# Optimization experiments

Hardware: AMD Instinct MI355X
Metric: run time of the kernel (lower is better)

The kernel has to match this reference:

```python
import jax, jax.numpy as jnp
import numpy as np

B, S, HID = 1, 4096, 2048
NH, NKV, D = 16, 4, 128
BLK, M, K_TOP = 64, 32, 8
THETA = 10000.0
NEG = jnp.float32(-1e9)


def setup_inputs() -> dict:
    key = jax.random.key(0)
    ks = jax.random.split(key, 6)
    s = 0.02
    return {
        "hidden_states": jax.random.normal(ks[0], (B, S, HID), jnp.float32),
        "position_ids": jnp.arange(S, dtype=jnp.int32)[None, :],
        "Wq": jax.random.normal(ks[1], (HID, NH * D), jnp.float32) * s,
        "Wk": jax.random.normal(ks[2], (HID, NKV * D), jnp.float32) * s,
        "Wv": jax.random.normal(ks[3], (HID, NKV * D), jnp.float32) * s,
        "Wo": jax.random.normal(ks[4], (NH * D, HID), jnp.float32) * s,
        # seeded random-sign (Hadamard-style) sketch projection, non-trainable buffer
        "H_sketch": jnp.sign(jax.random.normal(ks[5], (D, M), jnp.float32)) / jnp.sqrt(jnp.float32(M)),
    }


def _rot_half(x):
    x1, x2 = x[..., : D // 2], x[..., D // 2 :]
    return jnp.concatenate([-x2, x1], axis=-1)


def reference(hidden_states, position_ids, Wq, Wk, Wv, Wo, H_sketch):
    # QKV projections -> [B, heads, S, D]
    q = (hidden_states @ Wq).reshape(B, S, NH, D).transpose(0, 2, 1, 3)
    k = (hidden_states @ Wk).reshape(B, S, NKV, D).transpose(0, 2, 1, 3)
    v = (hidden_states @ Wv).reshape(B, S, NKV, D).transpose(0, 2, 1, 3)

    # RoPE
    inv_freq = 1.0 / (THETA ** (jnp.arange(0, D, 2, dtype=jnp.float32) / D))
    freqs = position_ids.astype(jnp.float32)[:, :, None] * inv_freq[None, None, :]
    emb = jnp.concatenate([freqs, freqs], axis=-1)  # [B, S, D]
    cos, sin = jnp.cos(emb)[:, None], jnp.sin(emb)[:, None]  # [B, 1, S, D]
    q = q * cos + _rot_half(q) * sin
    k = k * cos + _rot_half(k) * sin

    # GQA repeat kv heads
    rep = NH // NKV
    k = jnp.repeat(k, rep, axis=1)
    v = jnp.repeat(v, rep, axis=1)

    nblk = S // BLK
    # Hadamard-sketch projections, block-mean pooled -> [B, NH, nblk, M]
    Sq = jnp.einsum("bhsd,dm->bhsm", q, H_sketch).reshape(B, NH, nblk, BLK, M).mean(axis=3)
    Sk = jnp.einsum("bhsd,dm->bhsm", k, H_sketch).reshape(B, NH, nblk, BLK, M).mean(axis=3)

    # Block-level sketch scores, causal at block granularity, diagonal forced in
    bs = jnp.einsum("bhim,bhjm->bhij", Sq, Sk)
    blk_causal = jnp.tril(jnp.ones((nblk, nblk), dtype=bool))
    bs = jnp.where(blk_causal, bs, NEG)
    bs = jnp.where(jnp.eye(nblk, dtype=bool), jnp.float32(1e9), bs)
    _, idx = jax.lax.top_k(bs, K_TOP)  # [B, NH, nblk, K_TOP]

    # Gather selected K/V blocks -> [B, NH, nblk, K_TOP, BLK, D]
    K5 = k.reshape(B, NH, nblk, BLK, D)
    V5 = v.reshape(B, NH, nblk, BLK, D)
    gidx = idx[..., None, None]
    Kg = jnp.take_along_axis(K5[:, :, None], gidx, axis=3)
    Vg = jnp.take_along_axis(V5[:, :, None], gidx, axis=3)

    # Block-sparse scores [B, NH, nblk, BLK, K_TOP, BLK]
    Qb = q.reshape(B, NH, nblk, BLK, D)
    scores = jnp.einsum("bhnqd,bhnkcd->bhnqkc", Qb, Kg) / jnp.sqrt(jnp.float32(D))

    # Token-level causal mask over gathered keys
    qpos = jnp.arange(nblk)[:, None] * BLK + jnp.arange(BLK)[None, :]  # [nblk, BLK]
    kpos = idx[..., None] * BLK + jnp.arange(BLK)  # [B, NH, nblk, K_TOP, BLK]
    mask = kpos[:, :, :, None] <= qpos[None, None, :, :, None, None]
    scores = jnp.where(mask, scores, NEG)

    probs = jax.nn.softmax(scores.reshape(B, NH, nblk, BLK, K_TOP * BLK), axis=-1)
    probs = probs.reshape(scores.shape)

    out = jnp.einsum("bhnqkc,bhnkcd->bhnqd", probs, Vg)
    out = out.reshape(B, NH, S, D).transpose(0, 2, 1, 3).reshape(B, S, NH * D)
    return out @ Wo
```

## Files before the change

kernel.cpp:

```cpp
#include <hip/hip_runtime.h>
#include <hip/hip_bf16.h>

#define S_LEN 4096
#define HID 2048
#define NH 16
#define NKV 4
#define HD 128
#define MSK 32
#define KTOP 8
#define NBLK 64
#define NEGV -1000000000.0f
#define SENT -3.0e38f

typedef __hip_bfloat16 bf16;
typedef __attribute__((ext_vector_type(8))) short short8;
typedef __attribute__((ext_vector_type(4))) float f32x4;


__device__ __forceinline__ unsigned short f2b(float v) {
    __hip_bfloat16 h = __float2bfloat16(v);
    return *reinterpret_cast<unsigned short*>(&h);
}
__device__ __forceinline__ float b2f(unsigned short u) {
    return __bfloat162float(*reinterpret_cast<__hip_bfloat16*>(&u));
}
__device__ __forceinline__ void gl16(const void* g, void* l) {
    __builtin_amdgcn_global_load_lds(
        (const __attribute__((address_space(1))) void*)g,
        (__attribute__((address_space(3))) void*)l, 16, 0, 0);
}

__global__ __launch_bounds__(256) void prepass(
    const float* __restrict__ Wq, const float* __restrict__ Wk,
    const float* __restrict__ Wv, const float* __restrict__ Wo,
    const float* __restrict__ A,
    bf16* __restrict__ WtqH, bf16* __restrict__ WtqL,
    bf16* __restrict__ WtkH, bf16* __restrict__ WtkL,
    bf16* __restrict__ WtvH, bf16* __restrict__ WtoH,
    bf16* __restrict__ AhiT, bf16* __restrict__ AloT,
    int nA) {
    __shared__ __align__(16) float LsArena[64 * 68];
    const int t = threadIdx.x;
    int bx = blockIdx.x;

    if (bx < nA) {
        const int rb = bx >> 6, kt = bx & 63;
        char* DH = (char*)AhiT + ((size_t)rb * 64 + kt) * 8192;
        char* DL = (char*)AloT + ((size_t)rb * 64 + kt) * 8192;
#pragma unroll
        for (int i = 0; i < 2; i++) {
            const int task = t + i * 256;
            const int row = task >> 2, lq = task & 3;
            const float* ap = &A[(size_t)(rb * 128 + row) * HID + kt * 32 + lq * 8];
            const float4 v0 = *(const float4*)ap;
            const float4 v1 = *(const float4*)(ap + 4);
            const float f[8] = {v0.x, v0.y, v0.z, v0.w, v1.x, v1.y, v1.z, v1.w};
            alignas(16) unsigned short hh[8], lo[8];
#pragma unroll
            for (int j = 0; j < 8; j++) {
                hh[j] = f2b(f[j]);
                lo[j] = f2b(f[j] - b2f(hh[j]));
            }
            const size_t off = (size_t)(((row * 4 + lq) ^ (row & 7))) * 16;
            *(uint4*)(DH + off) = *(const uint4*)hh;
            *(uint4*)(DL + off) = *(const uint4*)lo;
        }
        return;
    }
    bx -= nA;

    if (bx < 1536) {
        const int u = bx >> 6, kt = bx & 63, k0 = kt * 32;
        const float* W; char* TH; char* TL; int Nd, n0; bool hasLo;
        if (u < 16)      { W = Wq; TH = (char*)WtqH + (size_t)u * 524288;        TL = (char*)WtqL + (size_t)u * 524288; Nd = 2048; n0 = u * 128; hasLo = true; }
        else if (u < 20) { W = Wk; TH = (char*)WtkH + (size_t)(u - 16) * 524288; TL = (char*)WtkL + (size_t)(u - 16) * 524288; Nd = 512; n0 = (u - 16) * 128; hasLo = true; }
        else             { W = Wv; TH = (char*)WtvH + (size_t)(u - 20) * 524288; TL = nullptr; Nd = 512; n0 = (u - 20) * 128; hasLo = false; }
        float(*Lw)[132] = (float(*)[132])LsArena;
#pragma unroll
        for (int i = 0; i < 4; i++) {
            const int task = t + i * 256;
            const int k = task >> 5, c4 = task & 31;
            *(float4*)&Lw[k][c4 * 4] = *(const float4*)&W[(size_t)(k0 + k) * Nd + n0 + c4 * 4];
        }
        __syncthreads();
#pragma unroll
        for (int i = 0; i < 2; i++) {
            const int task = t + i * 256;
            const int col = task >> 2, lq = task & 3;
            alignas(16) unsigned short hh[8], lo[8];
#pragma unroll
            for (int j = 0; j < 8; j++) {
                const float x = Lw[lq * 8 + j][col];
                hh[j] = f2b(x);
                lo[j] = f2b(x - b2f(hh[j]));
            }
            const size_t off = (size_t)kt * 8192 + (size_t)(((col * 4 + lq) ^ (col & 7))) * 16;
            *(uint4*)(TH + off) = *(const uint4*)hh;
            if (hasLo) *(uint4*)(TL + off) = *(const uint4*)lo;
        }
        return;
    }
    bx -= 1536;

    {
        const int n0 = (bx >> 5) * 64, k0 = (bx & 31) * 64;
        float(*Ls)[68] = (float(*)[68])LsArena;
        {
            const int kk = t >> 2, c0 = (t & 3) * 16;
#pragma unroll
            for (int i = 0; i < 4; i++)
                *(float4*)&Ls[kk][c0 + i * 4] =
                    *(const float4*)&Wo[(size_t)(k0 + kk) * HID + n0 + c0 + i * 4];
        }
        __syncthreads();
        const int c = t >> 2, ks = (t & 3) * 16;
        alignas(16) unsigned short hh[16];
#pragma unroll
        for (int j = 0; j < 16; j++) hh[j] = f2b(Ls[ks + j][c]);
        unsigned short* TH = (unsigned short*)WtoH;
        const size_t db = (size_t)(n0 + c) * HID + k0 + ks;
        *(uint4*)&TH[db + 0] = *(const uint4*)&hh[0];
        *(uint4*)&TH[db + 8] = *(const uint4*)&hh[8];
    }
}

__global__ __launch_bounds__(256, 3) void proj4(
    const float* __restrict__ A,
    const bf16* __restrict__ AhiT_, const bf16* __restrict__ AloT_,
    const bf16* __restrict__ WtqH_, const bf16* __restrict__ WtqL_,
    const bf16* __restrict__ WtkH_, const bf16* __restrict__ WtkL_,
    const bf16* __restrict__ WtvH_,
    const int* __restrict__ pos_ids, const float* __restrict__ H,
    bf16* __restrict__ qf, bf16* __restrict__ kf, bf16* __restrict__ vfT,
    float* __restrict__ Sq, float* __restrict__ Sk) {
    const int u = blockIdx.x;
    const int rb = blockIdx.y;
    const bool isQ = (u < 16);
    const bool isV = (u >= 20);
    const bool np3 = !isV;
    const int h = isQ ? u : (isV ? (u - 20) : (u - 16));
    const char* WHb = (const char*)(isQ ? WtqH_ : (isV ? WtvH_ : WtkH_)) + (size_t)h * 524288;
    const char* WLb = (const char*)(isQ ? WtqL_ : WtkL_) + (size_t)h * 524288;
    const char* AHb = (const char*)AhiT_;
    const char* ALb = (const char*)AloT_;
    bf16* __restrict__ Xout = isQ ? qf : kf;
    float* __restrict__ Sout = isQ ? Sq : Sk;
    const int Nd = isQ ? (NH * HD) : (NKV * HD);

    const int m0g = rb * 128;
    const int t = threadIdx.x;
    const int w = t >> 6, L = t & 63;
    const int lm = L & 15, lq = L >> 4;

    __shared__ __align__(16) char arena[34816];
    __shared__ float red[4][128];
    char* Wh_s = arena;
    char* Wl_s = arena + 8192;
    char* Ah_s = arena + 16384;
    char* Al_s = arena + 24576;

    f32x4 acc[2][8];
#pragma unroll
    for (int mt = 0; mt < 2; mt++)
#pragma unroll
        for (int nt = 0; nt < 8; nt++) acc[mt][nt] = (f32x4){0.f, 0.f, 0.f, 0.f};

    for (int kt = 0; kt < 64; kt++) {
        __syncthreads();
        const size_t tW = (size_t)kt * 8192;
#pragma unroll
        for (int i = 0; i < 2; i++) {
            const int so = (w * 2 + i) * 1024;
            gl16(WHb + tW + so + L * 16, Wh_s + so);
            if (np3) gl16(WLb + tW + so + L * 16, Wl_s + so);
        }
        if (AHb) {
            const size_t tA = ((size_t)rb * 64 + kt) * 8192;
#pragma unroll
            for (int i = 0; i < 2; i++) {
                const int so = (w * 2 + i) * 1024;
                gl16(AHb + tA + so + L * 16, Ah_s + so);
                if (np3) gl16(ALb + tA + so + L * 16, Al_s + so);
            }
        } else {
            const int k0 = kt * 32;
#pragma unroll
            for (int i = 0; i < 2; i++) {
                const int task = t + i * 256;
                const int row = task >> 2, q2 = task & 3;
                const float* ap = &A[(size_t)(m0g + row) * HID + k0 + q2 * 8];
                const float4 v0 = *(const float4*)ap;
                const float4 v1 = *(const float4*)(ap + 4);
                const float f[8] = {v0.x, v0.y, v0.z, v0.w, v1.x, v1.y, v1.z, v1.w};
                alignas(16) unsigned short hh[8], lo[8];
#pragma unroll
                for (int j = 0; j < 8; j++) {
                    hh[j] = f2b(f[j]);
                    if (np3) lo[j] = f2b(f[j] - b2f(hh[j]));
                }
                const int ch = ((row * 4 + q2) ^ (row & 7)) * 16;
                *(uint4*)(Ah_s + ch) = *(const uint4*)hh;
                if (np3) *(uint4*)(Al_s + ch) = *(const uint4*)lo;
            }
        }
        __syncthreads();
        const int xr = lm & 7;
        short8 ah[2], al[2];
#pragma unroll
        for (int mt = 0; mt < 2; mt++) {
            const int rowA = w * 32 + mt * 16 + lm;
            const int cA = (((rowA * 4 + lq) ^ xr)) * 16;
            ah[mt] = *(const short8*)(Ah_s + cA);
            if (np3) al[mt] = *(const short8*)(Al_s + cA);
        }
#pragma unroll
        for (int nt = 0; nt < 8; nt++) {
            const int rowW = nt * 16 + lm;
            const int cW = (((rowW * 4 + lq) ^ xr)) * 16;
            const short8 bh = *(const short8*)(Wh_s + cW);
#pragma unroll
            for (int mt = 0; mt < 2; mt++)
                acc[mt][nt] = __builtin_amdgcn_mfma_f32_16x16x32_bf16(ah[mt], bh, acc[mt][nt], 0, 0, 0);
            if (np3) {
                const short8 bl = *(const short8*)(Wl_s + cW);
#pragma unroll
                for (int mt = 0; mt < 2; mt++) {
                    acc[mt][nt] = __builtin_amdgcn_mfma_f32_16x16x32_bf16(ah[mt], bl, acc[mt][nt], 0, 0, 0);
                    acc[mt][nt] = __builtin_amdgcn_mfma_f32_16x16x32_bf16(al[mt], bh, acc[mt][nt], 0, 0, 0);
                }
            }
        }
    }

    if (isV) {
        __syncthreads();
        unsigned short(*Tv)[136] = (unsigned short(*)[136])arena;
#pragma unroll
        for (int mt = 0; mt < 2; mt++) {
            const int rbs = w * 32 + mt * 16 + lq * 4;
#pragma unroll
            for (int rr = 0; rr < 4; rr++)
#pragma unroll
                for (int nt = 0; nt < 8; nt++)
                    Tv[nt * 16 + lm][rbs + rr] = f2b(acc[mt][nt][rr]);
        }
        __syncthreads();
        const int col = t >> 1, rh = (t & 1) * 64;
        bf16* dst = &vfT[((size_t)h * HD + col) * S_LEN + m0g + rh];
#pragma unroll
        for (int u2 = 0; u2 < 8; u2++)
            *(uint4*)&dst[u2 * 8] = *(const uint4*)&Tv[col][rh + u2 * 8];
        return;
    }

    {
        float invf[4];
#pragma unroll
        for (int c4 = 0; c4 < 4; c4++) {
            const int jj = c4 * 16 + lm;
            invf[c4] = 1.0f / powf(10000.0f, (float)jj * (1.0f / 64.0f));
        }
#pragma unroll
        for (int mt = 0; mt < 2; mt++) {
            const int rbase = w * 32 + mt * 16 + lq * 4;
#pragma unroll
            for (int rr = 0; rr < 4; rr++) {
                const float p = (float)pos_ids[m0g + rbase + rr];
#pragma unroll
                for (int c4 = 0; c4 < 4; c4++) {
                    const float fr = p * invf[c4];
                    float sv, cv;
                    sincosf(fr, &sv, &cv);
                    const float x1 = acc[mt][c4][rr];
                    const float x2 = acc[mt][c4 + 4][rr];
                    acc[mt][c4][rr]     = x1 * cv - x2 * sv;
                    acc[mt][c4 + 4][rr] = x2 * cv + x1 * sv;
                }
            }
        }
    }

    float cs[8];
#pragma unroll
    for (int nt = 0; nt < 8; nt++) cs[nt] = 0.f;
#pragma unroll
    for (int mt = 0; mt < 2; mt++) {
        const int rbase = w * 32 + mt * 16 + lq * 4;
#pragma unroll
        for (int rr = 0; rr < 4; rr++) {
            bf16* dst = &Xout[(size_t)(m0g + rbase + rr) * Nd + h * HD + lm];
#pragma unroll
            for (int nt = 0; nt < 8; nt++) {
                const float v = acc[mt][nt][rr];
                dst[nt * 16] = __float2bfloat16(v);
                cs[nt] += v;
            }
        }
    }
#pragma unroll
    for (int nt = 0; nt < 8; nt++) {
        cs[nt] += __shfl_xor(cs[nt], 16);
        cs[nt] += __shfl_xor(cs[nt], 32);
    }
    if (lq == 0) {
#pragma unroll
        for (int nt = 0; nt < 8; nt++) red[w][nt * 16 + lm] = cs[nt];
    }
    __syncthreads();
    if (t < 64) {
        const int b = t >> 5, m = t & 31;
        float s = 0.f;
        for (int d = 0; d < 128; d++)
            s += (red[b * 2][d] + red[b * 2 + 1][d]) * H[d * MSK + m];
        Sout[((size_t)h * NBLK + (m0g >> 6) + b) * MSK + m] = s * (1.0f / 64.0f);
    }
}

__global__ __launch_bounds__(256, 3) void proj_rope_sketch(
    const float* __restrict__ A, const float* __restrict__ Wq,
    const float* __restrict__ Wk, const float* __restrict__ Wv,
    const int* __restrict__ pos_ids, const float* __restrict__ H,
    bf16* __restrict__ qf, bf16* __restrict__ kf, bf16* __restrict__ vf,
    float* __restrict__ Sq, float* __restrict__ Sk,
    int u0, int r0, int xbase) {
    const int u = blockIdx.x + u0;
    const bool isQ = (u < 16);
    const bool isV = (u >= 20);
    const bool np3 = !isV;
    const int h = isQ ? u : (isV ? (u - 20) : (u - 16));
    const float* __restrict__ W = isQ ? Wq : (isV ? Wv : Wk);
    const int Nd = isQ ? (NH * HD) : (NKV * HD);
    bf16* __restrict__ Xout = isQ ? qf : kf;
    float* __restrict__ Sout = isQ ? Sq : Sk;

    const int m0g = r0 + blockIdx.y * 128;
    const int m0x = isQ ? (m0g - xbase) : m0g;
    const int t = threadIdx.x;
    const int w = t >> 6, L = t & 63;
    const int lm = L & 15, lq = L >> 4;

    __shared__ __align__(16) unsigned short shmem[4 * 128 * 40];
    __shared__ float red[4][128];
    unsigned short(*pAh)[40] = (unsigned short(*)[40])(shmem);
    unsigned short(*pAl)[40] = (unsigned short(*)[40])(shmem + 128 * 40);
    unsigned short(*pWh)[40] = (unsigned short(*)[40])(shmem + 2 * 128 * 40);
    unsigned short(*pWl)[40] = (unsigned short(*)[40])(shmem + 3 * 128 * 40);

    f32x4 acc[2][8];
#pragma unroll
    for (int mt = 0; mt < 2; mt++)
#pragma unroll
        for (int nt = 0; nt < 8; nt++) acc[mt][nt] = (f32x4){0.f, 0.f, 0.f, 0.f};

    for (int k0 = 0; k0 < HID; k0 += 32) {
        __syncthreads();
#pragma unroll
        for (int i = 0; i < 4; i++) {
            const int idx = t + i * 256;
            const int row = idx >> 3, f4 = idx & 7;
            const float4 v = *(const float4*)&A[(size_t)(m0g + row) * HID + k0 + f4 * 4];
            ushort4 uh;
            uh.x = f2b(v.x); uh.y = f2b(v.y); uh.z = f2b(v.z); uh.w = f2b(v.w);
            *(ushort4*)&pAh[row][f4 * 4] = uh;
            if (np3) {
                ushort4 ul;
                ul.x = f2b(v.x - b2f(uh.x)); ul.y = f2b(v.y - b2f(uh.y));
                ul.z = f2b(v.z - b2f(uh.z)); ul.w = f2b(v.w - b2f(uh.w));
                *(ushort4*)&pAl[row][f4 * 4] = ul;
            }
        }
        {
            const int wcol = t >> 1, wk0 = (t & 1) * 16;
            const float* wp = &W[(size_t)(k0 + wk0) * Nd + h * HD + wcol];
            alignas(16) unsigned short hh[16];
            alignas(16) unsigned short ll[16];
#pragma unroll
            for (int uu = 0; uu < 16; uu++) {
                const float x = wp[(size_t)uu * Nd];
                hh[uu] = f2b(x);
                ll[uu] = f2b(x - b2f(hh[uu]));
            }
            *(uint4*)&pWh[wcol][wk0 + 0] = *(const uint4*)&hh[0];
            *(uint4*)&pWh[wcol][wk0 + 8] = *(const uint4*)&hh[8];
            if (np3) {
                *(uint4*)&pWl[wcol][wk0 + 0] = *(const uint4*)&ll[0];
                *(uint4*)&pWl[wcol][wk0 + 8] = *(const uint4*)&ll[8];
            }
        }
        __syncthreads();
        short8 ah[2], al[2];
#pragma unroll
        for (int mt = 0; mt < 2; mt++) {
            ah[mt] = *(const short8*)&pAh[w * 32 + mt * 16 + lm][lq * 8];
            if (np3) al[mt] = *(const short8*)&pAl[w * 32 + mt * 16 + lm][lq * 8];
        }
#pragma unroll
        for (int nt = 0; nt < 8; nt++) {
            const short8 bh = *(const short8*)&pWh[nt * 16 + lm][lq * 8];
#pragma unroll
            for (int mt = 0; mt < 2; mt++)
                acc[mt][nt] = __builtin_amdgcn_mfma_f32_16x16x32_bf16(ah[mt], bh, acc[mt][nt], 0, 0, 0);
            if (np3) {
                const short8 bl = *(const short8*)&pWl[nt * 16 + lm][lq * 8];
#pragma unroll
                for (int mt = 0; mt < 2; mt++) {
                    acc[mt][nt] = __builtin_amdgcn_mfma_f32_16x16x32_bf16(ah[mt], bl, acc[mt][nt], 0, 0, 0);
                    acc[mt][nt] = __builtin_amdgcn_mfma_f32_16x16x32_bf16(al[mt], bh, acc[mt][nt], 0, 0, 0);
                }
            }
        }
    }

    if (isV) {
        __syncthreads();
        unsigned short(*Tv)[136] = (unsigned short(*)[136])shmem;
#pragma unroll
        for (int mt = 0; mt < 2; mt++) {
            const int rbs = w * 32 + mt * 16 + lq * 4;
#pragma unroll
            for (int rr = 0; rr < 4; rr++)
#pragma unroll
                for (int nt = 0; nt < 8; nt++)
                    Tv[nt * 16 + lm][rbs + rr] = f2b(acc[mt][nt][rr]);
        }
        __syncthreads();
        const int col = t >> 1, rh = (t & 1) * 64;
        bf16* dst = &vf[((size_t)h * HD + col) * S_LEN + m0g + rh];
#pragma unroll
        for (int u2 = 0; u2 < 8; u2++)
            *(uint4*)&dst[u2 * 8] = *(const uint4*)&Tv[col][rh + u2 * 8];
        return;
    }

    {
        float invf[4];
#pragma unroll
        for (int c4 = 0; c4 < 4; c4++) {
            const int jj = c4 * 16 + lm;
            invf[c4] = 1.0f / powf(10000.0f, (float)jj * (1.0f / 64.0f));
        }
#pragma unroll
        for (int mt = 0; mt < 2; mt++) {
            const int rbase = w * 32 + mt * 16 + lq * 4;
#pragma unroll
            for (int rr = 0; rr < 4; rr++) {
                const float p = (float)pos_ids[m0g + rbase + rr];
#pragma unroll
                for (int c4 = 0; c4 < 4; c4++) {
                    const float fr = p * invf[c4];
                    float sv, cv;
                    sincosf(fr, &sv, &cv);
                    const float x1 = acc[mt][c4][rr];
                    const float x2 = acc[mt][c4 + 4][rr];
                    acc[mt][c4][rr]     = x1 * cv - x2 * sv;
                    acc[mt][c4 + 4][rr] = x2 * cv + x1 * sv;
                }
            }
        }
    }

    float cs[8];
#pragma unroll
    for (int nt = 0; nt < 8; nt++) cs[nt] = 0.f;
#pragma unroll
    for (int mt = 0; mt < 2; mt++) {
        const int rbase = w * 32 + mt * 16 + lq * 4;
#pragma unroll
        for (int rr = 0; rr < 4; rr++) {
            bf16* dst = &Xout[(size_t)(m0x + rbase + rr) * Nd + h * HD + lm];
#pragma unroll
            for (int nt = 0; nt < 8; nt++) {
                const float v = acc[mt][nt][rr];
                dst[nt * 16] = __float2bfloat16(v);
                cs[nt] += v;
            }
        }
    }
#pragma unroll
    for (int nt = 0; nt < 8; nt++) {
        cs[nt] += __shfl_xor(cs[nt], 16);
        cs[nt] += __shfl_xor(cs[nt], 32);
    }
    if (lq == 0) {
#pragma unroll
        for (int nt = 0; nt < 8; nt++) red[w][nt * 16 + lm] = cs[nt];
    }
    __syncthreads();
    if (t < 64) {
        const int b = t >> 5, m = t & 31;
        float s = 0.f;
        for (int d = 0; d < 128; d++)
            s += (red[b * 2][d] + red[b * 2 + 1][d]) * H[d * MSK + m];
        Sout[((size_t)h * NBLK + (m0g >> 6) + b) * MSK + m] = s * (1.0f / 64.0f);
    }
}

__global__ __launch_bounds__(64) void topk_kernel(const float* __restrict__ Sq,
                                                  const float* __restrict__ Sk,
                                                  int* __restrict__ topk, int i0) {
    const int i = i0 + blockIdx.x, h = blockIdx.y, kv = h >> 2;
    const int j = threadIdx.x;
    __shared__ float vals[64];
    float v;
    if (j > i) v = NEGV;
    else if (j == i) v = 1e9f;
    else {
        v = 0.f;
        const float* sq = Sq + ((size_t)h * NBLK + i) * MSK;
        const float* sk = Sk + ((size_t)kv * NBLK + j) * MSK;
        for (int m = 0; m < MSK; m++) v += sq[m] * sk[m];
    }
    vals[j] = v;
    __syncthreads();
    if (j == 0) {
        for (int kk = 0; kk < KTOP; kk++) {
            float best = SENT; int bi = 0;
            for (int jj = 0; jj < 64; jj++)
                if (vals[jj] > best) { best = vals[jj]; bi = jj; }
            vals[bi] = SENT;
            topk[((size_t)h * NBLK + i) * KTOP + kk] = bi;
        }
    }
}

__global__ __launch_bounds__(256) void attn_kernel(bf16* __restrict__ qf,
                                                   const bf16* __restrict__ kf,
                                                   const bf16* __restrict__ vfT,
                                                   const int* __restrict__ topk,
                                                   const float* __restrict__ Sq,
                                                   const float* __restrict__ Sk,
                                                   int r0, int qbase) {
    const int qbg = (r0 >> 6) + blockIdx.x;
    const int h = blockIdx.y, kvh = h >> 2;
    const int t = threadIdx.x;
    const int w = t >> 6, L = t & 63;
    const int lm = L & 15, lq = L >> 4;

    __shared__ __align__(16) unsigned short Ks[64][136];
    __shared__ __align__(16) unsigned short Vt[128][72];
    __shared__ __align__(16) unsigned short Ps[64][72];
    __shared__ int selS[KTOP];

    if (Sq != nullptr) {
        if (w == 0) {
            const int j = L;
            float v;
            if (j > qbg) v = NEGV;
            else if (j == qbg) v = 1e9f;
            else {
                v = 0.f;
                const float* sq = Sq + ((size_t)h * NBLK + qbg) * MSK;
                const float* sk = Sk + ((size_t)kvh * NBLK + j) * MSK;
                for (int m = 0; m < MSK; m++) v += sq[m] * sk[m];
            }
#pragma unroll
            for (int kk = 0; kk < KTOP; kk++) {
                float bv = v; int bi = j;
#pragma unroll
                for (int d = 1; d < 64; d <<= 1) {
                    const float ov = __shfl_xor(bv, d);
                    const int oi = __shfl_xor(bi, d);
                    if (ov > bv || (ov == bv && oi < bi)) { bv = ov; bi = oi; }
                }
                if (j == bi) v = SENT;
                if (j == 0) selS[kk] = bi;
            }
        }
    } else if (t < KTOP) {
        selS[t] = topk[((size_t)h * NBLK + qbg) * KTOP + t];
    }

    short8 qfrag[4];
    {
        const size_t qrow = (size_t)(qbg * 64 - qbase) + w * 16 + lm;
        const unsigned short* qp = (const unsigned short*)qf + qrow * (NH * HD) + h * HD;
#pragma unroll
        for (int ks = 0; ks < 4; ks++)
            qfrag[ks] = *(const short8*)&qp[ks * 32 + lq * 8];
    }
    f32x4 O[8];
#pragma unroll
    for (int nt = 0; nt < 8; nt++) O[nt] = (f32x4){0.f, 0.f, 0.f, 0.f};
    f32x4 mrow = (f32x4){-1e30f, -1e30f, -1e30f, -1e30f};
    f32x4 lrow = (f32x4){0.f, 0.f, 0.f, 0.f};

    const int qpos0 = qbg * 64 + w * 16 + lq * 4;
    const float scale = 0.08838834764831845f;

    for (int kb = 0; kb < KTOP; kb++) {
        __syncthreads();
        const int blk = selS[kb] & 63;
#pragma unroll
        for (int i = 0; i < 4; i++) {
            const int idx = t + i * 256;
            const int rr = idx >> 4, c8 = idx & 15;
            *(uint4*)&Ks[rr][c8 * 8] =
                *(const uint4*)&kf[(size_t)(blk * 64 + rr) * (NKV * HD) + kvh * HD + c8 * 8];
        }
#pragma unroll
        for (int i = 0; i < 4; i++) {
            const int idx = t + i * 256;
            const int dd = idx >> 3, j8 = idx & 7;
            *(uint4*)&Vt[dd][j8 * 8] =
                *(const uint4*)&vfT[((size_t)kvh * HD + dd) * S_LEN + blk * 64 + j8 * 8];
        }
        __syncthreads();
        f32x4 S4[4];
#pragma unroll
        for (int nt = 0; nt < 4; nt++) {
            S4[nt] = (f32x4){0.f, 0.f, 0.f, 0.f};
#pragma unroll
            for (int ks = 0; ks < 4; ks++) {
                const short8 bk = *(const short8*)&Ks[nt * 16 + lm][ks * 32 + lq * 8];
                S4[nt] = __builtin_amdgcn_mfma_f32_16x16x32_bf16(qfrag[ks], bk, S4[nt], 0, 0, 0);
            }
        }
#pragma unroll
        for (int nt = 0; nt < 4; nt++) {
            const int kpos = blk * 64 + nt * 16 + lm;
#pragma unroll
            for (int r = 0; r < 4; r++)
                S4[nt][r] = (kpos <= qpos0 + r) ? S4[nt][r] * scale : NEGV;
        }
        f32x4 mx = S4[0];
#pragma unroll
        for (int nt = 1; nt < 4; nt++)
#pragma unroll
            for (int r = 0; r < 4; r++) mx[r] = fmaxf(mx[r], S4[nt][r]);
#pragma unroll
        for (int d = 1; d < 16; d <<= 1)
#pragma unroll
            for (int r = 0; r < 4; r++) mx[r] = fmaxf(mx[r], __shfl_xor(mx[r], d));
        f32x4 mnew, alv, sum;
#pragma unroll
        for (int r = 0; r < 4; r++) {
            mnew[r] = fmaxf(mrow[r], mx[r]);
            alv[r] = __expf(mrow[r] - mnew[r]);
            sum[r] = 0.f;
        }
#pragma unroll
        for (int nt = 0; nt < 4; nt++)
#pragma unroll
            for (int r = 0; r < 4; r++) {
                const float p = __expf(S4[nt][r] - mnew[r]);
                S4[nt][r] = p;
                sum[r] += p;
            }
#pragma unroll
        for (int d = 1; d < 16; d <<= 1)
#pragma unroll
            for (int r = 0; r < 4; r++) sum[r] += __shfl_xor(sum[r], d);
#pragma unroll
        for (int r = 0; r < 4; r++) {
            lrow[r] = lrow[r] * alv[r] + sum[r];
            mrow[r] = mnew[r];
        }
#pragma unroll
        for (int nt = 0; nt < 4; nt++)
#pragma unroll
            for (int r = 0; r < 4; r++)
                Ps[w * 16 + lq * 4 + r][nt * 16 + lm] = f2b(S4[nt][r]);
#pragma unroll
        for (int nt = 0; nt < 8; nt++)
#pragma unroll
            for (int r = 0; r < 4; r++) O[nt][r] *= alv[r];
#pragma unroll
        for (int ks2 = 0; ks2 < 2; ks2++) {
            const short8 pa = *(const short8*)&Ps[w * 16 + lm][ks2 * 32 + lq * 8];
#pragma unroll
            for (int nt = 0; nt < 8; nt++) {
                const short8 vv = *(const short8*)&Vt[nt * 16 + lm][ks2 * 32 + lq * 8];
                O[nt] = __builtin_amdgcn_mfma_f32_16x16x32_bf16(pa, vv, O[nt], 0, 0, 0);
            }
        }
    }
    f32x4 inv;
#pragma unroll
    for (int r = 0; r < 4; r++) inv[r] = 1.0f / lrow[r];
    const size_t orow0 = (size_t)(qbg * 64 - qbase) + w * 16 + lq * 4;
#pragma unroll
    for (int nt = 0; nt < 8; nt++)
#pragma unroll
        for (int r = 0; r < 4; r++)
            qf[(orow0 + r) * (NH * HD) + h * HD + nt * 16 + lm] =
                __float2bfloat16(O[nt][r] * inv[r]);
}

__global__ __launch_bounds__(256) void gemm_out(const bf16* __restrict__ A,
                                                const float* __restrict__ W,
                                                float* __restrict__ C, int cRow0) {
    __shared__ __align__(16) unsigned short Wl[128][40];
    const int n0 = blockIdx.x * 128, m0 = blockIdx.y * 128;
    const int t = threadIdx.x;
    const int w = t >> 6, L = t & 63;
    const int lm = L & 15, lq = L >> 4;
    const int wcol = t >> 1, wk0 = (t & 1) * 16;
    f32x4 acc[2][8];
#pragma unroll
    for (int mt = 0; mt < 2; mt++)
#pragma unroll
        for (int nt = 0; nt < 8; nt++) acc[mt][nt] = (f32x4){0.f, 0.f, 0.f, 0.f};

    float wreg[16];
    {
        const float* wp = &W[(size_t)wk0 * HID + n0 + wcol];
#pragma unroll
        for (int u = 0; u < 16; u++) wreg[u] = wp[(size_t)u * HID];
    }
    short8 av[2];
#pragma unroll
    for (int mt = 0; mt < 2; mt++)
        av[mt] = *(const short8*)&A[(size_t)(m0 + w * 32 + mt * 16 + lm) * HID + lq * 8];

    for (int k0 = 0; k0 < HID; k0 += 32) {
        __syncthreads();
        {
            alignas(16) unsigned short hh[16];
#pragma unroll
            for (int u = 0; u < 16; u++) hh[u] = f2b(wreg[u]);
            *(uint4*)&Wl[wcol][wk0 + 0] = *(const uint4*)&hh[0];
            *(uint4*)&Wl[wcol][wk0 + 8] = *(const uint4*)&hh[8];
        }
        const int k1 = k0 + 32;
        if (k1 < HID) {
            const float* wp = &W[(size_t)(k1 + wk0) * HID + n0 + wcol];
#pragma unroll
            for (int u = 0; u < 16; u++) wreg[u] = wp[(size_t)u * HID];
        }
        __syncthreads();
        short8 avn[2];
        if (k1 < HID) {
#pragma unroll
            for (int mt = 0; mt < 2; mt++)
                avn[mt] = *(const short8*)&A[(size_t)(m0 + w * 32 + mt * 16 + lm) * HID + k1 + lq * 8];
        }
#pragma unroll
        for (int nt = 0; nt < 8; nt++) {
            const short8 bv = *(const short8*)&Wl[nt * 16 + lm][lq * 8];
#pragma unroll
            for (int mt = 0; mt < 2; mt++)
                acc[mt][nt] = __builtin_amdgcn_mfma_f32_16x16x32_bf16(av[mt], bv, acc[mt][nt], 0, 0, 0);
        }
        if (k1 < HID) { av[0] = avn[0]; av[1] = avn[1]; }
    }
#pragma unroll
    for (int mt = 0; mt < 2; mt++)
#pragma unroll
        for (int nt = 0; nt < 8; nt++)
#pragma unroll
            for (int r = 0; r < 4; r++) {
                const int row = m0 + w * 32 + mt * 16 + lq * 4 + r;
                C[(size_t)(cRow0 + row) * HID + n0 + nt * 16 + lm] = acc[mt][nt][r];
            }
}

__global__ __launch_bounds__(256) void gemm_out2(const bf16* __restrict__ A,
                                                 const bf16* __restrict__ WtoH,
                                                 float* __restrict__ C) {
    __shared__ __align__(16) unsigned short Wl[128][72];
    const int n0 = blockIdx.x * 128, m0 = blockIdx.y * 128;
    const int t = threadIdx.x;
    const int w = t >> 6, L = t & 63;
    const int lm = L & 15, lq = L >> 4;
    const int ct = t >> 1, sg = (t & 1) * 32;
    const unsigned short* __restrict__ WT = (const unsigned short*)WtoH;
    f32x4 acc[2][8];
#pragma unroll
    for (int mt = 0; mt < 2; mt++)
#pragma unroll
        for (int nt = 0; nt < 8; nt++) acc[mt][nt] = (f32x4){0.f, 0.f, 0.f, 0.f};

    uint4 wbuf[4];
    {
        const unsigned short* wp = &WT[(size_t)(n0 + ct) * HID + sg];
#pragma unroll
        for (int i = 0; i < 4; i++) wbuf[i] = *(const uint4*)&wp[i * 8];
    }
    short8 av[2][2];
#pragma unroll
    for (int mt = 0; mt < 2; mt++)
#pragma unroll
        for (int ks = 0; ks < 2; ks++)
            av[mt][ks] = *(const short8*)&A[(size_t)(m0 + w * 32 + mt * 16 + lm) * HID + ks * 32 + lq * 8];

    for (int k0 = 0; k0 < HID; k0 += 64) {
        __syncthreads();
#pragma unroll
        for (int i = 0; i < 4; i++) *(uint4*)&Wl[ct][sg + i * 8] = wbuf[i];
        const int k1 = k0 + 64;
        if (k1 < HID) {
            const unsigned short* wp = &WT[(size_t)(n0 + ct) * HID + k1 + sg];
#pragma unroll
            for (int i = 0; i < 4; i++) wbuf[i] = *(const uint4*)&wp[i * 8];
        }
        __syncthreads();
        short8 avn[2][2];
        if (k1 < HID) {
#pragma unroll
            for (int mt = 0; mt < 2; mt++)
#pragma unroll
                for (int ks = 0; ks < 2; ks++)
                    avn[mt][ks] = *(const short8*)&A[(size_t)(m0 + w * 32 + mt * 16 + lm) * HID + k1 + ks * 32 + lq * 8];
        }
#pragma unroll
        for (int ks = 0; ks < 2; ks++)
#pragma unroll
            for (int nt = 0; nt < 8; nt++) {
                const short8 bv = *(const short8*)&Wl[nt * 16 + lm][ks * 32 + lq * 8];
#pragma unroll
                for (int mt = 0; mt < 2; mt++)
                    acc[mt][nt] = __builtin_amdgcn_mfma_f32_16x16x32_bf16(av[mt][ks], bv, acc[mt][nt], 0, 0, 0);
            }
        if (k1 < HID) {
#pragma unroll
            for (int mt = 0; mt < 2; mt++)
#pragma unroll
                for (int ks = 0; ks < 2; ks++) av[mt][ks] = avn[mt][ks];
        }
    }
#pragma unroll
    for (int mt = 0; mt < 2; mt++)
#pragma unroll
        for (int nt = 0; nt < 8; nt++)
#pragma unroll
            for (int r = 0; r < 4; r++) {
                const int row = m0 + w * 32 + mt * 16 + lq * 4 + r;
                C[(size_t)row * HID + n0 + nt * 16 + lm] = acc[mt][nt][r];
            }
}

extern "C" void kernel_launch(void* const* d_in, const int* in_sizes, int n_in,
                              void* d_out, int out_size, void* d_ws, size_t ws_size,
                              hipStream_t stream) {
    const void *p_hid, *p_pos, *p_wq, *p_wk, *p_wv, *p_wo, *p_h;
    if (in_sizes[0] == 4096 && in_sizes[1] == 1048576) {
        p_h = d_in[0]; p_wk = d_in[1]; p_wo = d_in[2]; p_wq = d_in[3];
        p_wv = d_in[4]; p_hid = d_in[5]; p_pos = d_in[6];
    } else {
        p_hid = d_in[0]; p_pos = d_in[1]; p_wq = d_in[2]; p_wk = d_in[3];
        p_wv = d_in[4]; p_wo = d_in[5]; p_h = d_in[6];
    }
    const float* hidden = (const float*)p_hid;
    const int* pos_ids  = (const int*)p_pos;
    const float* Wq = (const float*)p_wq;
    const float* Wk = (const float*)p_wk;
    const float* Wv = (const float*)p_wv;
    const float* Wo = (const float*)p_wo;
    const float* Hsk = (const float*)p_h;
    float* out = (float*)d_out;

    char* base = (char*)d_ws;
    float* Sq    = (float*)base;
    float* Sk    = (float*)(base + 131072);
    int*   topkb = (int*)(base + 163840);
    bf16*  kf    = (bf16*)(base + 196608);
    bf16*  vfT   = (bf16*)(base + 196608 + 4194304);
    bf16*  qbuf  = (bf16*)(base + 196608 + 8388608);
    bf16*  WtqH  = (bf16*)(base + 25362432);
    bf16*  WtqL  = (bf16*)(base + 33751040);
    bf16*  WtkH  = (bf16*)(base + 42139648);
    bf16*  WtkL  = (bf16*)(base + 44236800);
    bf16*  WtvH  = (bf16*)(base + 46333952);
    bf16*  WtoH  = (bf16*)(base + 48431104);
    bf16*  AhiT  = (bf16*)(base + 56819712);
    bf16*  AloT  = (bf16*)(base + 73596928);
    const size_t FULL_NEED  = 25362432;
    const size_t FULL2_NEED = 48431104;
    const size_t FULL3_NEED = 56819712;
    const size_t FULL4_NEED = 90374144;

    if (ws_size >= FULL2_NEED) {
        const bool hasWo = (ws_size >= FULL3_NEED);
        const bool hasA  = (ws_size >= FULL4_NEED);
        const int nA  = hasA ? 2048 : 0;
        const int nWo = hasWo ? 1024 : 0;
        prepass<<<dim3(nA + 1536 + nWo), 256, 0, stream>>>(
            Wq, Wk, Wv, Wo, hidden,
            WtqH, WtqL, WtkH, WtkL, WtvH, WtoH, AhiT, AloT, nA);
        proj4<<<dim3(24, 32), 256, 0, stream>>>(
            hidden, hasA ? AhiT : nullptr, hasA ? AloT : nullptr,
            WtqH, WtqL, WtkH, WtkL, WtvH, pos_ids, Hsk,
            qbuf, kf, vfT, Sq, Sk);
        attn_kernel<<<dim3(NBLK, NH), 256, 0, stream>>>(
            qbuf, kf, vfT, nullptr, Sq, Sk, 0, 0);
        if (hasWo)
            gemm_out2<<<dim3(HID / 128, S_LEN / 128), 256, 0, stream>>>(
                qbuf, WtoH, out);
        else
            gemm_out<<<dim3(HID / 128, S_LEN / 128), 256, 0, stream>>>(
                qbuf, Wo, out, 0);
    } else if (ws_size >= FULL_NEED) {
        proj_rope_sketch<<<dim3(24, S_LEN / 128), 256, 0, stream>>>(
            hidden, Wq, Wk, Wv, pos_ids, Hsk, qbuf, kf, vfT, Sq, Sk, 0, 0, 0);
        attn_kernel<<<dim3(NBLK, NH), 256, 0, stream>>>(
            qbuf, kf, vfT, nullptr, Sq, Sk, 0, 0);
        gemm_out<<<dim3(HID / 128, S_LEN / 128), 256, 0, stream>>>(
            qbuf, Wo, out, 0);
    } else {
        proj_rope_sketch<<<dim3(8, S_LEN / 128), 256, 0, stream>>>(
            hidden, Wq, Wk, Wv, pos_ids, Hsk, qbuf, kf, vfT, Sq, Sk, 16, 0, 0);
        for (int c = 0; c < 16; c++) {
            const int r0 = c * 256;
            proj_rope_sketch<<<dim3(16, 2), 256, 0, stream>>>(
                hidden, Wq, Wk, Wv, pos_ids, Hsk, qbuf, kf, vfT, Sq, Sk, 0, r0, r0);
            topk_kernel<<<dim3(4, NH), 64, 0, stream>>>(Sq, Sk, topkb, r0 >> 6);
            attn_kernel<<<dim3(4, NH), 256, 0, stream>>>(
                qbuf, kf, vfT, topkb, nullptr, nullptr, r0, r0);
            gemm_out<<<dim3(HID / 128, 2), 256, 0, stream>>>(
                qbuf, Wo, out, r0);
        }
    }
}
```

Before: 443.8 us.

## Coalesce attention output stores via LDS and stage A tiles through shared memory

The attention kernel's epilogue now writes normalized bf16 outputs into the shared Ks tile first, then stores rows to global memory with 16-byte coalesced writes instead of scattered 2-byte stores. The output projection GEMM now loads A tiles cooperatively into a new LDS buffer with coalesced 16-byte global loads, rather than each lane fetching its MFMA fragments straight from global memory. Both changes aim to cut uncoalesced global traffic. The cost is extra barriers and more LDS use, which could reduce occupancy.

```diff
diff --git a/kernel.cpp b/kernel.cpp
--- a/kernel.cpp
+++ b/kernel.cpp
@@ -677,13 +677,23 @@
     f32x4 inv;
 #pragma unroll
     for (int r = 0; r < 4; r++) inv[r] = 1.0f / lrow[r];
-    const size_t orow0 = (size_t)(qbg * 64 - qbase) + w * 16 + lq * 4;
+    __syncthreads();
 #pragma unroll
     for (int nt = 0; nt < 8; nt++)
 #pragma unroll
         for (int r = 0; r < 4; r++)
-            qf[(orow0 + r) * (NH * HD) + h * HD + nt * 16 + lm] =
-                __float2bfloat16(O[nt][r] * inv[r]);
+            Ks[w * 16 + lq * 4 + r][nt * 16 + lm] = f2b(O[nt][r] * inv[r]);
+    __syncthreads();
+    {
+        const size_t orow0 = (size_t)(qbg * 64 - qbase);
+#pragma unroll
+        for (int i = 0; i < 4; i++) {
+            const int idx = t + i * 256;
+            const int row = idx >> 4, c8 = idx & 15;
+            *(uint4*)&qf[(orow0 + row) * (NH * HD) + h * HD + c8 * 8] =
+                *(const uint4*)&Ks[row][c8 * 8];
+        }
+    }
 }
 
 __global__ __launch_bounds__(256) void gemm_out(const bf16* __restrict__ A,
@@ -758,11 +768,13 @@
                                                  const bf16* __restrict__ WtoH,
                                                  float* __restrict__ C) {
     __shared__ __align__(16) unsigned short Wl[128][72];
+    __shared__ __align__(16) unsigned short Al[128][72];
     const int n0 = blockIdx.x * 128, m0 = blockIdx.y * 128;
     const int t = threadIdx.x;
     const int w = t >> 6, L = t & 63;
     const int lm = L & 15, lq = L >> 4;
     const int ct = t >> 1, sg = (t & 1) * 32;
+    const int ar = t >> 1, ag = (t & 1) * 4;
     const unsigned short* __restrict__ WT = (const unsigned short*)WtoH;
     f32x4 acc[2][8];
 #pragma unroll
@@ -770,52 +782,45 @@
 #pragma unroll
         for (int nt = 0; nt < 8; nt++) acc[mt][nt] = (f32x4){0.f, 0.f, 0.f, 0.f};
 
-    uint4 wbuf[4];
+    uint4 wbuf[4], abuf[4];
     {
         const unsigned short* wp = &WT[(size_t)(n0 + ct) * HID + sg];
 #pragma unroll
         for (int i = 0; i < 4; i++) wbuf[i] = *(const uint4*)&wp[i * 8];
-    }
-    short8 av[2][2];
-#pragma unroll
-    for (int mt = 0; mt < 2; mt++)
-#pragma unroll
-        for (int ks = 0; ks < 2; ks++)
-            av[mt][ks] = *(const short8*)&A[(size_t)(m0 + w * 32 + mt * 16 + lm) * HID + ks * 32 + lq * 8];
+        const unsigned short* apg = (const unsigned short*)A + (size_t)(m0 + ar) * HID + ag * 8;
+#pragma unroll
+        for (int i = 0; i < 4; i++) abuf[i] = *(const uint4*)&apg[i * 8];
+    }
 
     for (int k0 = 0; k0 < HID; k0 += 64) {
         __syncthreads();
 #pragma unroll
         for (int i = 0; i < 4; i++) *(uint4*)&Wl[ct][sg + i * 8] = wbuf[i];
+#pragma unroll
+        for (int i = 0; i < 4; i++) *(uint4*)&Al[ar][ag * 8 + i * 8] = abuf[i];
         const int k1 = k0 + 64;
         if (k1 < HID) {
             const unsigned short* wp = &WT[(size_t)(n0 + ct) * HID + k1 + sg];
 #pragma unroll
             for (int i = 0; i < 4; i++) wbuf[i] = *(const uint4*)&wp[i * 8];
-        }
-        __syncthreads();
-        short8 avn[2][2];
-        if (k1 < HID) {
+            const unsigned short* apg = (const unsigned short*)A + (size_t)(m0 + ar) * HID + k1 + ag * 8;
+#pragma unroll
+            for (int i = 0; i < 4; i++) abuf[i] = *(const uint4*)&apg[i * 8];
+        }
+        __syncthreads();
+#pragma unroll
+        for (int ks = 0; ks < 2; ks++) {
+            short8 av[2];
 #pragma unroll
             for (int mt = 0; mt < 2; mt++)
-#pragma unroll
-                for (int ks = 0; ks < 2; ks++)
-                    avn[mt][ks] = *(const short8*)&A[(size_t)(m0 + w * 32 + mt * 16 + lm) * HID + k1 + ks * 32 + lq * 8];
-        }
-#pragma unroll
-        for (int ks = 0; ks < 2; ks++)
+                av[mt] = *(const short8*)&Al[w * 32 + mt * 16 + lm][ks * 32 + lq * 8];
 #pragma unroll
             for (int nt = 0; nt < 8; nt++) {
                 const short8 bv = *(const short8*)&Wl[nt * 16 + lm][ks * 32 + lq * 8];
 #pragma unroll
                 for (int mt = 0; mt < 2; mt++)
-                    acc[mt][nt] = __builtin_amdgcn_mfma_f32_16x16x32_bf16(av[mt][ks], bv, acc[mt][nt], 0, 0, 0);
-            }
-        if (k1 < HID) {
-#pragma unroll
-            for (int mt = 0; mt < 2; mt++)
-#pragma unroll
-                for (int ks = 0; ks < 2; ks++) av[mt][ks] = avn[mt][ks];
+                    acc[mt][nt] = __builtin_amdgcn_mfma_f32_16x16x32_bf16(av[mt], bv, acc[mt][nt], 0, 0, 0);
+            }
         }
     }
 #pragma unroll
```

New measurement: 501.5 us. +13.0%, slower.
